# Performance work log

Measured on AMD Instinct MI355X. Metric: run time of the kernel, lower is better.

Reference implementation:

```python
import jax, jax.numpy as jnp
import numpy as np

DIMS = 1024
BATCH, SEQ = 4, 2048

def setup_inputs() -> dict:
    key = jax.random.key(0)
    k1, k2, k3, k4 = jax.random.split(key, 4)
    scale = 1.0 / np.sqrt(DIMS)
    return {
        "input_seq_embs": jax.random.normal(k1, (BATCH, SEQ, DIMS), dtype=jnp.float32),
        "Wq": jax.random.normal(k2, (DIMS, DIMS), dtype=jnp.float32) * scale,
        "Wk": jax.random.normal(k3, (DIMS, DIMS), dtype=jnp.float32) * scale,
        "Wv": jax.random.normal(k4, (DIMS, DIMS), dtype=jnp.float32) * scale,
    }

def reference(input_seq_embs, Wq, Wk, Wv):
    # nn.Linear(x) = x @ W.T ; weights stored [out, in]
    q = jnp.einsum('bsd,ed->bse', input_seq_embs, Wq)
    k = jnp.einsum('bsd,ed->bse', input_seq_embs, Wk)
    v = jnp.einsum('bsd,ed->bse', input_seq_embs, Wv)
    # full N x N scores, NO 1/sqrt(d) scaling (faithful to source)
    scores = jnp.einsum('bqe,bke->bqk', q, k)
    causal = jnp.tril(jnp.ones((q.shape[1], q.shape[1]), dtype=bool))
    scores = jnp.where(causal[None, :, :], scores, -jnp.inf)
    attn = jax.nn.softmax(scores, axis=-1)
    return jnp.einsum('bqk,bke->bqe', attn, v)
```

## Files before the change

kernel.cpp:

```cpp
#include <hip/hip_runtime.h>


typedef _Float16 h8 __attribute__((ext_vector_type(8)));
typedef _Float16 h4 __attribute__((ext_vector_type(4)));
typedef float f32x4 __attribute__((ext_vector_type(4)));

#define BM 128
#define BN 128

__device__ __forceinline__ void gl_lds16(const _Float16* g, _Float16* l) {
    __builtin_amdgcn_global_load_lds(
        (const __attribute__((address_space(1))) void*)g,
        (__attribute__((address_space(3))) void*)l, 16, 0, 0);
}

#define BARX do { asm volatile("" ::: "memory"); __builtin_amdgcn_s_barrier(); \
                  asm volatile("" ::: "memory"); } while (0)
#define VMW(n) asm volatile("s_waitcnt vmcnt(" #n ")" ::: "memory")


#define SA_LO(gp, ab) do { gl_lds16((gp),          (ab) + wv * 1024); \
                           gl_lds16((gp) + 8192,   (ab) + wv * 1024 + 512); } while (0)
#define SA_HI(gp, ab) do { gl_lds16((gp) + 131072, (ab) + wv * 1024 + 8192); \
                           gl_lds16((gp) + 139264, (ab) + wv * 1024 + 8704); } while (0)
#define SB_LO(gp, bb) do { gl_lds16((gp),          (bb) + wv * 1024); \
                           gl_lds16((gp) + 8192,   (bb) + wv * 1024 + 512); } while (0)
#define SB_HI(gp2, bb)     gl_lds16((gp2),         (bb) + 8192 + wv * 512)

#define LDA(ab, h, ap) do { _Pragma("unroll") \
    for (int i = 0; i < 4; i++) \
        af[i] = *(const h8*)&(ab)[abase + (h) * 4096 + i * 1024 + (ap)]; } while (0)
#define LDB(bb, ap) do { _Pragma("unroll") \
    for (int j = 0; j < 3; j++) \
        bf[j] = *(const h8*)&(bb)[bbase + j * 1024 + (ap)]; } while (0)

#define MMP(h) do { __builtin_amdgcn_s_setprio(1); _Pragma("unroll") \
    for (int i = 0; i < 4; i++) { _Pragma("unroll") \
        for (int j = 0; j < 3; j++) \
            acc[(h) * 4 + i][j] = __builtin_amdgcn_mfma_f32_16x16x32_f16( \
                af[i], bf[j], acc[(h) * 4 + i][j], 0, 0, 0); } \
    __builtin_amdgcn_s_setprio(0); } while (0)

__global__ __launch_bounds__(512, 2) void qkv192(
    const _Float16* __restrict__ A, const _Float16* __restrict__ B,
    _Float16* __restrict__ C)
{
    __shared__ __align__(16) _Float16 sm[73728];

    const int bid = blockIdx.x;
    const int wg = (bid & 7) * 64 + (bid >> 3);
    const int by = wg >> 4, bx = wg & 15;
    const int m0 = by * 256, n0 = bx * 192;

    const int tid = threadIdx.x;
    const int l = tid & 63;
    const int wv = tid >> 6;

    const int prow = wv * 16 + (l >> 3);
    const int pseg = ((l & 7) ^ ((l >> 3) & 7)) * 8;
    const _Float16* gA  = A + (size_t)(m0 + prow) * 1024 + pseg;
    const _Float16* gB  = B + (size_t)(n0 + prow) * 1024 + pseg;
    const _Float16* gB2 = B + (size_t)(n0 + 128 + wv * 8 + (l >> 3)) * 1024 + pseg;

    const int la = l & 15, qd = l >> 4;
    const int wmr = (wv >> 2) * 128;
    const int wnr = (wv & 3) * 48;
    const int ap0 = ((qd) ^ (la & 7)) * 8;
    const int ap1 = ((4 + qd) ^ (la & 7)) * 8;
    const int abase = (wmr + la) * 64;
    const int bbase = (wnr + la) * 64;

    _Float16* a0 = sm;
    _Float16* a1 = sm + 16384;
    _Float16* a2 = sm + 32768;
    _Float16* b0 = sm + 49152;
    _Float16* b1 = sm + 61440;

    f32x4 acc[8][3];
    #pragma unroll
    for (int i = 0; i < 8; i++)
        #pragma unroll
        for (int j = 0; j < 3; j++)
            acc[i][j] = (f32x4){0.f, 0.f, 0.f, 0.f};

    SA_LO(gA, a0);      SA_HI(gA, a0);
    SB_LO(gB, b0);      SB_HI(gB2, b0);
    SA_LO(gA + 64, a1); SA_HI(gA + 64, a1);
    VMW(4);
    BARX;

    const _Float16* pA  = gA + 128;
    const _Float16* pB  = gB + 64;
    const _Float16* pB2 = gB2 + 64;

    #pragma unroll 1
    for (int n = 0; n < 14; ++n) {
        h8 af[4], bf[3];
        LDB(b0, ap0); LDA(a0, 0, ap0); SB_LO(pB, b1);  BARX; MMP(0); BARX;
        LDA(a0, 1, ap0);               SB_HI(pB2, b1); BARX; MMP(1); BARX;
        LDB(b0, ap1); LDA(a0, 0, ap1); SA_LO(pA, a2);  BARX; MMP(0); BARX;
        LDA(a0, 1, ap1);               SA_HI(pA, a2);  BARX; MMP(1); VMW(4); BARX;
        _Float16* t = a0; a0 = a1; a1 = a2; a2 = t;
        t = b0; b0 = b1; b1 = t;
        pA += 64; pB += 64; pB2 += 64;
    }
    {
        h8 af[4], bf[3];
        LDB(b0, ap0); LDA(a0, 0, ap0); SB_LO(pB, b1);  BARX; MMP(0); BARX;
        LDA(a0, 1, ap0);               SB_HI(pB2, b1); BARX; MMP(1); BARX;
        LDB(b0, ap1); LDA(a0, 0, ap1);                 BARX; MMP(0); BARX;
        LDA(a0, 1, ap1);                               BARX; MMP(1); VMW(0); BARX;
        _Float16* t = a0; a0 = a1; a1 = a2; a2 = t;
        t = b0; b0 = b1; b1 = t;
    }
    {
        h8 af[4], bf[3];
        LDB(b0, ap0); LDA(a0, 0, ap0); BARX; MMP(0); BARX;
        LDA(a0, 1, ap0);               BARX; MMP(1); BARX;
        LDB(b0, ap1); LDA(a0, 0, ap1); BARX; MMP(0); BARX;
        LDA(a0, 1, ap1);               BARX; MMP(1);
    }

    #pragma unroll
    for (int i = 0; i < 8; i++) {
        const int m = m0 + wmr + i * 16 + qd * 4;
        #pragma unroll
        for (int j = 0; j < 3; j++) {
            const int col16 = n0 + wnr + j * 16;
            const int slab = col16 >> 10;
            if (slab < 2) {
                const size_t base = (size_t)slab * 8388608 + (col16 & 1023) + la;
                #pragma unroll
                for (int rr = 0; rr < 4; rr++)
                    C[base + (size_t)(m + rr) * 1024] = (_Float16)acc[i][j][rr];
            } else {
                _Float16* Vt = C + (size_t)2 * 8388608;
                const int e = col16 + la - 2048;
                const int b = m >> 11;
                const int sl = m & 2047;
                h4 vv = { (_Float16)acc[i][j][0], (_Float16)acc[i][j][1],
                          (_Float16)acc[i][j][2], (_Float16)acc[i][j][3] };
                *(h4*)(Vt + (size_t)b * 2097152 + (size_t)e * 2048 + sl) = vv;
            }
        }
    }
}

template<int SWZ, int OM, bool KLIM>
__global__ __launch_bounds__(256) void gemm_nt(
    const _Float16* __restrict__ A, const _Float16* __restrict__ B,
    void* __restrict__ Cp, int N, int K,
    size_t sAz, size_t sBz, size_t sCz)
{
    __shared__ __align__(16) char smem[32768];
    _Float16* As = (_Float16*)smem;
    _Float16* Bs = (_Float16*)(smem + 16384);

    int bx, by;
    if (SWZ == 1) {
        const int r = blockIdx.x & 7, q2 = blockIdx.x >> 3;
        bx = q2 >> 3;
        by = ((q2 & 7) << 3) | r;
    } else if (SWZ == 2) {
        const int r = blockIdx.x & 7, g = blockIdx.x >> 3;
        if (g <= r) { by = r;      bx = g; }
        else        { by = 15 - r; bx = g - (r + 1); }
    } else {
        const int r = blockIdx.x & 7, g = blockIdx.x >> 3;
        by = (g & 1) ? (15 - r) : r;
        bx = g >> 1;
    }

    const int tid  = threadIdx.x;
    const int lane = tid & 63;
    const int wv   = tid >> 6;
    const int m0 = by * BM, n0 = bx * BN;
    const size_t z = blockIdx.z;

    const int lr = lane >> 2;
    const int lc = ((lane & 3) ^ ((lane >> 3) & 3)) * 8;
    const _Float16* pA0 = A + z * sAz + (size_t)(m0 + wv * 16 + lr) * K + lc;
    const _Float16* pA1 = pA0 + (size_t)64 * K;
    const _Float16* pB0 = B + z * sBz + (size_t)(n0 + wv * 16 + lr) * K + lc;
    const _Float16* pB1 = pB0 + (size_t)64 * K;
    _Float16* lA0 = As + wv * 512;
    _Float16* lA1 = As + (wv + 4) * 512;
    _Float16* lB0 = Bs + wv * 512;
    _Float16* lB1 = Bs + (wv + 4) * 512;

    const int la = lane & 15;
    const int qd = lane >> 4;
    const int wm = (wv >> 1) * 64;
    const int wn = (wv & 1) * 64;
    const int sg = (qd ^ ((la >> 1) & 3)) * 8;

    f32x4 acc[4][4];
    #pragma unroll
    for (int i = 0; i < 4; i++)
        #pragma unroll
        for (int j = 0; j < 4; j++)
            acc[i][j] = (f32x4){0.f, 0.f, 0.f, 0.f};

    const int kEnd = KLIM ? (m0 + BM) : K;

    for (int k0 = 0; k0 < kEnd; k0 += 64) {
        gl_lds16(pA0,      lA0);
        gl_lds16(pA1,      lA1);
        gl_lds16(pB0,      lB0);
        gl_lds16(pB1,      lB1);
        gl_lds16(pA0 + 32, lA0 + 4096);
        gl_lds16(pA1 + 32, lA1 + 4096);
        gl_lds16(pB0 + 32, lB0 + 4096);
        gl_lds16(pB1 + 32, lB1 + 4096);
        pA0 += 64; pA1 += 64; pB0 += 64; pB1 += 64;
        __syncthreads();

        #pragma unroll
        for (int s = 0; s < 2; s++) {
            h8 af[4], bf[4];
            #pragma unroll
            for (int i = 0; i < 4; i++)
                af[i] = *(const h8*)&As[s * 4096 + (wm + i * 16 + la) * 32 + sg];
            #pragma unroll
            for (int i = 0; i < 4; i++)
                bf[i] = *(const h8*)&Bs[s * 4096 + (wn + i * 16 + la) * 32 + sg];
            #pragma unroll
            for (int i = 0; i < 4; i++)
                #pragma unroll
                for (int j = 0; j < 4; j++)
                    acc[i][j] = __builtin_amdgcn_mfma_f32_16x16x32_f16(af[i], bf[j], acc[i][j], 0, 0, 0);
        }
        __syncthreads();
    }

    if (OM == 2) {
        _Float16* C = (_Float16*)Cp;
        if (n0 < 2048) {
            #pragma unroll
            for (int i = 0; i < 4; i++)
                #pragma unroll
                for (int j = 0; j < 4; j++) {
                    const int col  = n0 + wn + j * 16 + la;
                    const size_t base = (size_t)(col >> 10) * 8388608 + (col & 1023);
                    #pragma unroll
                    for (int rr = 0; rr < 4; rr++)
                        C[base + (size_t)(m0 + wm + i * 16 + qd * 4 + rr) * 1024] =
                            (_Float16)acc[i][j][rr];
                }
        } else {
            _Float16* Vt = C + (size_t)2 * 8388608;
            #pragma unroll
            for (int i = 0; i < 4; i++) {
                const int m  = m0 + wm + i * 16 + qd * 4;
                const int b  = m >> 11;
                const int sl = m & 2047;
                _Float16* Vb = Vt + (size_t)b * 2097152 + sl;
                #pragma unroll
                for (int j = 0; j < 4; j++) {
                    const int e = n0 - 2048 + wn + j * 16 + la;
                    h4 vv = { (_Float16)acc[i][j][0], (_Float16)acc[i][j][1],
                              (_Float16)acc[i][j][2], (_Float16)acc[i][j][3] };
                    *(h4*)(Vb + (size_t)e * 2048) = vv;
                }
            }
        }
    } else {
        float* C = (float*)Cp + z * sCz;
        #pragma unroll
        for (int i = 0; i < 4; i++)
            #pragma unroll
            for (int j = 0; j < 4; j++)
                #pragma unroll
                for (int rr = 0; rr < 4; rr++)
                    C[(size_t)(m0 + wm + i * 16 + qd * 4 + rr) * N + (n0 + wn + j * 16 + la)] =
                        acc[i][j][rr];
    }
}

__global__ __launch_bounds__(256) void cvt_all(
    const float* __restrict__ x, const float* __restrict__ Wq,
    const float* __restrict__ Wk, const float* __restrict__ Wv,
    _Float16* __restrict__ x_h, _Float16* __restrict__ Wh)
{
    const int bid = blockIdx.x;
    const float* src; _Float16* dst; size_t off;
    if (bid < 4096) {
        src = x; dst = x_h; off = (size_t)bid * 2048;
    } else {
        const int b2 = bid - 4096;
        const int w = b2 >> 9;
        src = (w == 0) ? Wq : ((w == 1) ? Wk : Wv);
        dst = Wh + (size_t)w * 1048576;
        off = (size_t)(b2 & 511) * 2048;
    }
    const size_t i = off + (size_t)threadIdx.x * 8;
    float4 a = *(const float4*)(src + i);
    float4 b = *(const float4*)(src + i + 4);
    h8 o = { (_Float16)a.x, (_Float16)a.y, (_Float16)a.z, (_Float16)a.w,
             (_Float16)b.x, (_Float16)b.y, (_Float16)b.z, (_Float16)b.w };
    *(h8*)(dst + i) = o;
}

__global__ __launch_bounds__(256) void softmax_causal(const float* __restrict__ S,
                                                      _Float16* __restrict__ P)
{
    const int idx = blockIdx.x;
    const int q = idx & 2047;
    const float* Srow = S + (size_t)idx * 2048;
    _Float16* Prow = P + (size_t)idx * 2048;
    const int t = threadIdx.x;
    const int k0 = t * 8;
    const int lane = t & 63, wv = t >> 6;
    __shared__ float red[4];

    float v[8];
    const bool any = (k0 <= q);
    if (any) {
        float4 a = *(const float4*)(Srow + k0);
        float4 b = *(const float4*)(Srow + k0 + 4);
        v[0] = a.x; v[1] = a.y; v[2] = a.z; v[3] = a.w;
        v[4] = b.x; v[5] = b.y; v[6] = b.z; v[7] = b.w;
    }
    float mx = -3.4e38f;
    #pragma unroll
    for (int j = 0; j < 8; j++)
        if (any && k0 + j <= q) mx = fmaxf(mx, v[j]);
    #pragma unroll
    for (int o = 32; o > 0; o >>= 1) mx = fmaxf(mx, __shfl_down(mx, o, 64));
    if (lane == 0) red[wv] = mx;
    __syncthreads();
    const float mall = fmaxf(fmaxf(red[0], red[1]), fmaxf(red[2], red[3]));
    __syncthreads();

    float sum = 0.f;
    #pragma unroll
    for (int j = 0; j < 8; j++) {
        float e = (any && k0 + j <= q) ? __expf(v[j] - mall) : 0.f;
        v[j] = e;
        sum += e;
    }
    #pragma unroll
    for (int o = 32; o > 0; o >>= 1) sum += __shfl_down(sum, o, 64);
    if (lane == 0) red[wv] = sum;
    __syncthreads();
    const float inv = 1.f / (red[0] + red[1] + red[2] + red[3]);

    const int kceil = ((q >> 7) + 1) << 7;
    if (k0 < kceil) {
        h8 o = { (_Float16)(v[0] * inv), (_Float16)(v[1] * inv),
                 (_Float16)(v[2] * inv), (_Float16)(v[3] * inv),
                 (_Float16)(v[4] * inv), (_Float16)(v[5] * inv),
                 (_Float16)(v[6] * inv), (_Float16)(v[7] * inv) };
        *(h8*)(Prow + k0) = o;
    }
}

extern "C" void kernel_launch(void* const* d_in, const int* in_sizes, int n_in,
                              void* d_out, int out_size, void* d_ws, size_t ws_size,
                              hipStream_t stream) {
    const float* x  = (const float*)d_in[0];
    const float* Wq = (const float*)d_in[1];
    const float* Wk = (const float*)d_in[2];
    const float* Wv = (const float*)d_in[3];
    float* out = (float*)d_out;

    const size_t MiB = 1024 * 1024;
    char* ws = (char*)d_ws;
    _Float16* QKVh = (_Float16*)ws;
    _Float16* Vt   = QKVh + (size_t)2 * 8388608;
    float*    S    = (float*)(ws + 48 * MiB);
    _Float16* x_h  = (_Float16*)(ws + 48 * MiB);
    _Float16* Wh   = (_Float16*)(ws + 64 * MiB);
    _Float16* P    = (_Float16*)ws;

    const dim3 blk(256);

    cvt_all<<<dim3(5632), blk, 0, stream>>>(x, Wq, Wk, Wv, x_h, Wh);

    qkv192<<<dim3(512), dim3(512), 0, stream>>>(x_h, Wh, QKVh);

    gemm_nt<2, 0, false><<<dim3(136, 1, 4), blk, 0, stream>>>(
        QKVh, QKVh + 8388608, S, 2048, 1024,
        (size_t)2097152, (size_t)2097152, (size_t)4194304);

    softmax_causal<<<dim3(4 * 2048), blk, 0, stream>>>(S, P);

    gemm_nt<3, 0, true><<<dim3(128, 1, 4), blk, 0, stream>>>(
        P, Vt, out, 1024, 2048,
        (size_t)4194304, (size_t)2097152, (size_t)2097152);
}
```

Measured before the change: 237.4 us.

## Fuse softmax normalization into PV GEMM using precomputed row max and sum

The softmax kernel now only computes each row's max and inverse sum (rowstat) and no longer writes the fp16 probability matrix. A new pv_fused kernel reads fp32 scores directly, applies exp, scaling and the causal mask while staging the A tile into LDS, then runs the MFMA GEMM against V. This removes the P write and read round trip and one kernel's worth of traffic. In exchange, each score is re-exponentiated once per column block, fp32 scores carry twice the bytes of fp16 P, and the A-side loads are synchronous register loads rather than async global-to-LDS copies.

```diff
diff --git a/kernel.cpp b/kernel.cpp
--- a/kernel.cpp
+++ b/kernel.cpp
@@ -275,6 +275,109 @@
                     C[(size_t)(m0 + wm + i * 16 + qd * 4 + rr) * N + (n0 + wn + j * 16 + la)] =
                         acc[i][j][rr];
     }
+}
+
+__global__ __launch_bounds__(256) void pv_fused(
+    const float* __restrict__ S, const float2* __restrict__ MS,
+    const _Float16* __restrict__ V, float* __restrict__ C)
+{
+    __shared__ __align__(16) char smem[32768];
+    _Float16* As = (_Float16*)smem;
+    _Float16* Bs = (_Float16*)(smem + 16384);
+
+    const int r = blockIdx.x & 7, g = blockIdx.x >> 3;
+    const int by = (g & 1) ? (15 - r) : r;
+    const int bx = g >> 1;
+    const int m0 = by * BM, n0 = bx * BN;
+    const size_t z = blockIdx.z;
+
+    const int tid  = threadIdx.x;
+    const int lane = tid & 63;
+    const int wv   = tid >> 6;
+
+    const int arow = tid & 127;
+    const int astg = tid >> 7;
+    const float* Srow = S + z * 4194304 + (size_t)(m0 + arow) * 2048 + astg * 32;
+    const float2 ms = MS[z * 2048 + m0 + arow];
+    const int qrow = m0 + arow;
+    const int ax = (arow >> 1) & 3;
+    _Float16* Arow = As + astg * 4096 + arow * 32;
+
+    const int lr = lane >> 2;
+    const int lc = ((lane & 3) ^ ((lane >> 3) & 3)) * 8;
+    const _Float16* pB0 = V + z * 2097152 + (size_t)(n0 + wv * 16 + lr) * 2048 + lc;
+    const _Float16* pB1 = pB0 + (size_t)64 * 2048;
+    _Float16* lB0 = Bs + wv * 512;
+    _Float16* lB1 = Bs + (wv + 4) * 512;
+
+    const int la = lane & 15;
+    const int qd = lane >> 4;
+    const int wm = (wv >> 1) * 64;
+    const int wn = (wv & 1) * 64;
+    const int sg = (qd ^ ((la >> 1) & 3)) * 8;
+
+    f32x4 acc[4][4];
+    #pragma unroll
+    for (int i = 0; i < 4; i++)
+        #pragma unroll
+        for (int j = 0; j < 4; j++)
+            acc[i][j] = (f32x4){0.f, 0.f, 0.f, 0.f};
+
+    const int kEnd = m0 + BM;
+
+    #pragma unroll 1
+    for (int k0 = 0; k0 < kEnd; k0 += 64) {
+        gl_lds16(pB0,      lB0);
+        gl_lds16(pB1,      lB1);
+        gl_lds16(pB0 + 32, lB0 + 4096);
+        gl_lds16(pB1 + 32, lB1 + 4096);
+        pB0 += 64; pB1 += 64;
+
+        #pragma unroll
+        for (int gg = 0; gg < 4; gg++) {
+            const float4 a4 = *(const float4*)(Srow + k0 + gg * 8);
+            const float4 b4 = *(const float4*)(Srow + k0 + gg * 8 + 4);
+            const int kb = k0 + astg * 32 + gg * 8;
+            h8 pk;
+            pk[0] = (_Float16)((kb + 0 <= qrow) ? __expf(a4.x - ms.x) * ms.y : 0.f);
+            pk[1] = (_Float16)((kb + 1 <= qrow) ? __expf(a4.y - ms.x) * ms.y : 0.f);
+            pk[2] = (_Float16)((kb + 2 <= qrow) ? __expf(a4.z - ms.x) * ms.y : 0.f);
+            pk[3] = (_Float16)((kb + 3 <= qrow) ? __expf(a4.w - ms.x) * ms.y : 0.f);
+            pk[4] = (_Float16)((kb + 4 <= qrow) ? __expf(b4.x - ms.x) * ms.y : 0.f);
+            pk[5] = (_Float16)((kb + 5 <= qrow) ? __expf(b4.y - ms.x) * ms.y : 0.f);
+            pk[6] = (_Float16)((kb + 6 <= qrow) ? __expf(b4.z - ms.x) * ms.y : 0.f);
+            pk[7] = (_Float16)((kb + 7 <= qrow) ? __expf(b4.w - ms.x) * ms.y : 0.f);
+            *(h8*)(Arow + ((gg ^ ax) * 8)) = pk;
+        }
+        __syncthreads();
+
+        #pragma unroll
+        for (int s = 0; s < 2; s++) {
+            h8 af[4], bf[4];
+            #pragma unroll
+            for (int i = 0; i < 4; i++)
+                af[i] = *(const h8*)&As[s * 4096 + (wm + i * 16 + la) * 32 + sg];
+            #pragma unroll
+            for (int i = 0; i < 4; i++)
+                bf[i] = *(const h8*)&Bs[s * 4096 + (wn + i * 16 + la) * 32 + sg];
+            #pragma unroll
+            for (int i = 0; i < 4; i++)
+                #pragma unroll
+                for (int j = 0; j < 4; j++)
+                    acc[i][j] = __builtin_amdgcn_mfma_f32_16x16x32_f16(af[i], bf[j], acc[i][j], 0, 0, 0);
+        }
+        __syncthreads();
+    }
+
+    float* Cz = C + z * 2097152;
+    #pragma unroll
+    for (int i = 0; i < 4; i++)
+        #pragma unroll
+        for (int j = 0; j < 4; j++)
+            #pragma unroll
+            for (int rr = 0; rr < 4; rr++)
+                Cz[(size_t)(m0 + wm + i * 16 + qd * 4 + rr) * 1024 + (n0 + wn + j * 16 + la)] =
+                    acc[i][j][rr];
 }
 
 __global__ __launch_bounds__(256) void cvt_all(
@@ -301,13 +404,12 @@
     *(h8*)(dst + i) = o;
 }
 
-__global__ __launch_bounds__(256) void softmax_causal(const float* __restrict__ S,
-                                                      _Float16* __restrict__ P)
+__global__ __launch_bounds__(256) void rowstat(const float* __restrict__ S,
+                                               float2* __restrict__ MS)
 {
     const int idx = blockIdx.x;
     const int q = idx & 2047;
     const float* Srow = S + (size_t)idx * 2048;
-    _Float16* Prow = P + (size_t)idx * 2048;
     const int t = threadIdx.x;
     const int k0 = t * 8;
     const int lane = t & 63, wv = t >> 6;
@@ -336,22 +438,15 @@
     #pragma unroll
     for (int j = 0; j < 8; j++) {
         float e = (any && k0 + j <= q) ? __expf(v[j] - mall) : 0.f;
-        v[j] = e;
         sum += e;
     }
     #pragma unroll
     for (int o = 32; o > 0; o >>= 1) sum += __shfl_down(sum, o, 64);
     if (lane == 0) red[wv] = sum;
     __syncthreads();
-    const float inv = 1.f / (red[0] + red[1] + red[2] + red[3]);
-
-    const int kceil = ((q >> 7) + 1) << 7;
-    if (k0 < kceil) {
-        h8 o = { (_Float16)(v[0] * inv), (_Float16)(v[1] * inv),
-                 (_Float16)(v[2] * inv), (_Float16)(v[3] * inv),
-                 (_Float16)(v[4] * inv), (_Float16)(v[5] * inv),
-                 (_Float16)(v[6] * inv), (_Float16)(v[7] * inv) };
-        *(h8*)(Prow + k0) = o;
+    if (t == 0) {
+        const float inv = 1.f / (red[0] + red[1] + red[2] + red[3]);
+        MS[idx] = make_float2(mall, inv);
     }
 }
 
@@ -371,7 +466,7 @@
     float*    S    = (float*)(ws + 48 * MiB);
     _Float16* x_h  = (_Float16*)(ws + 48 * MiB);
     _Float16* Wh   = (_Float16*)(ws + 64 * MiB);
-    _Float16* P    = (_Float16*)ws;
+    float2*   MS   = (float2*)ws;
 
     const dim3 blk(256);
 
@@ -383,9 +478,7 @@
         QKVh, QKVh + 8388608, S, 2048, 1024,
         (size_t)2097152, (size_t)2097152, (size_t)4194304);
 
-    softmax_causal<<<dim3(4 * 2048), blk, 0, stream>>>(S, P);
-
-    gemm_nt<3, 0, true><<<dim3(128, 1, 4), blk, 0, stream>>>(
-        P, Vt, out, 1024, 2048,
-        (size_t)4194304, (size_t)2097152, (size_t)2097152);
-}
+    rowstat<<<dim3(4 * 2048), blk, 0, stream>>>(S, MS);
+
+    pv_fused<<<dim3(128, 1, 4), blk, 0, stream>>>(S, MS, Vt, out);
+}
```

After: 315.8 us. +33.0%, slower.
